# Optimization experiments

Measured on AMD Instinct MI355X. Metric: run time of the kernel, lower is better.

The kernel has to match this reference:

```python
import jax, jax.numpy as jnp
import numpy as np

H, HKV, D = 8, 1, 256  # query heads, kv heads, head_dim (Gemma-2B-like)


def apply_rope(x, sin, cos):
    # x: [B, h, D, S]; sin/cos: [B, 1, D//2, S]
    x1, x2 = jnp.split(x, 2, axis=-2)
    return jnp.concatenate((x1 * cos - x2 * sin, x2 * cos + x1 * sin), axis=-2)


def setup_inputs() -> dict:
    key = jax.random.key(0)
    ks = jax.random.split(key, 12)
    B, hidden, S = 2, 2048, 2048
    half = D // 2
    Xq = jax.random.normal(ks[0], (B, hidden, S), jnp.float32)
    Xkv = jax.random.normal(ks[1], (B, hidden, S), jnp.float32)
    sin_q = jax.random.uniform(ks[2], (B, 1, half, S), jnp.float32, -1.0, 1.0)
    cos_q = jax.random.uniform(ks[3], (B, 1, half, S), jnp.float32, -1.0, 1.0)
    sin_k = jax.random.uniform(ks[4], (B, 1, half, S), jnp.float32, -1.0, 1.0)
    cos_k = jax.random.uniform(ks[5], (B, 1, half, S), jnp.float32, -1.0, 1.0)
    attn_mask = jnp.zeros((B, 1, S, S), jnp.float32)
    scale = 0.02
    Wq = jax.random.normal(ks[6], (H * D, hidden), jnp.float32) * scale
    Wk = jax.random.normal(ks[7], (HKV * D, hidden), jnp.float32) * scale
    Wv = jax.random.normal(ks[8], (HKV * D, hidden), jnp.float32) * scale
    Wo = jax.random.normal(ks[9], (hidden, H * D), jnp.float32) * scale
    return {"Xq": Xq, "Xkv": Xkv, "sin_q": sin_q, "cos_q": cos_q,
            "sin_k": sin_k, "cos_k": cos_k, "attn_mask": attn_mask,
            "Wq": Wq, "Wk": Wk, "Wv": Wv, "Wo": Wo}


def reference(Xq, Xkv, sin_q, cos_q, sin_k, cos_k, attn_mask, Wq, Wk, Wv, Wo):
    B, hidden, Sq = Xq.shape
    Sk = Xkv.shape[-1]
    # ANEDenseGeneral = 1x1 conv over channels-first layout
    q = jnp.einsum('oc,bcs->bos', Wq, Xq).reshape(B, H, D, Sq)
    q = apply_rope(q, sin_q, cos_q)
    k = jnp.einsum('oc,bcs->bos', Wk, Xkv).reshape(B, HKV, D, Sk)
    k = apply_rope(k, sin_k, cos_k)
    v = jnp.einsum('oc,bcs->bos', Wv, Xkv).reshape(B, HKV, D, Sk)
    # GQA: broadcast kv heads to query heads
    rep = H // HKV
    k = jnp.repeat(k, rep, axis=1)
    v = jnp.repeat(v, rep, axis=1)
    scale = 1.0 / jnp.sqrt(jnp.asarray(D, Xq.dtype))
    scores = jnp.einsum('bhdq,bhdk->bhqk', q, k) * scale + attn_mask
    probs = jax.nn.softmax(scores, axis=-1)
    out = jnp.einsum('bhqk,bhdk->bhdq', probs, v).reshape(B, H * D, Sq)
    return jnp.einsum('oc,bcs->bos', Wo, out).astype(Xq.dtype)
```

## Files before the change

### kernel.cpp

```cpp
#include <hip/hip_runtime.h>

typedef __bf16 bf16;
typedef __bf16 bf16x8 __attribute__((ext_vector_type(8)));
typedef __bf16 bf16x4 __attribute__((ext_vector_type(4)));
typedef float f32x4 __attribute__((ext_vector_type(4)));

static constexpr int Hh = 8;
static constexpr int Dd = 256;
static constexpr int Ss = 2048;
static constexpr int Cc = 2048;
static constexpr int NS = 4096;

typedef const __attribute__((address_space(1))) unsigned int as1_u32;
typedef __attribute__((address_space(3))) unsigned int as3_u32;

__device__ __forceinline__ void gl_lds16(const void* g, void* l) {
  __builtin_amdgcn_global_load_lds((as1_u32*)(unsigned long long)g,
                                   (as3_u32*)(unsigned int)(unsigned long long)l,
                                   16, 0, 0);
}

__device__ __forceinline__ f32x4 mfma16(bf16x8 a, bf16x8 b, f32x4 c) {
  return __builtin_amdgcn_mfma_f32_16x16x32_bf16(a, b, c, 0, 0, 0);
}

__global__ __launch_bounds__(256) void cvt_w(const float* __restrict__ in,
                                             bf16* __restrict__ out, int n) {
  int i = (blockIdx.x * 256 + threadIdx.x) * 4;
  if (i >= n) return;
  const float4 v = *(const float4*)(in + i);
  bf16x4 o;
  o[0] = (bf16)v.x; o[1] = (bf16)v.y; o[2] = (bf16)v.z; o[3] = (bf16)v.w;
  *(bf16x4*)(out + i) = o;
}

__global__ __launch_bounds__(256) void transpose_cvt(const float* __restrict__ in,
                                                     bf16* __restrict__ out,
                                                     int R, int S) {
  __shared__ float t[32][33];
  const int b = blockIdx.z;
  const long base = (long)b * R * S;
  const int s0 = blockIdx.x * 32, r0 = blockIdx.y * 32;
  const int tx = threadIdx.x, ty = threadIdx.y;
#pragma unroll
  for (int i = 0; i < 32; i += 8)
    t[ty + i][tx] = in[base + (long)(r0 + ty + i) * S + s0 + tx];
  __syncthreads();
#pragma unroll
  for (int i = 0; i < 32; i += 8)
    out[base + (long)(s0 + ty + i) * R + r0 + tx] = (bf16)t[tx][ty + i];
}

__global__ __launch_bounds__(256) void transpose_cvt4(
    const float* __restrict__ s0, const float* __restrict__ s1,
    const float* __restrict__ s2, const float* __restrict__ s3,
    bf16* __restrict__ d0, bf16* __restrict__ d1, bf16* __restrict__ d2,
    bf16* __restrict__ d3, int R, int S) {
  __shared__ float t[32][33];
  const int arr = blockIdx.y >> 2;
  const int r0 = (blockIdx.y & 3) * 32;
  const float* in = (arr == 0) ? s0 : (arr == 1) ? s1 : (arr == 2) ? s2 : s3;
  bf16* out = (arr == 0) ? d0 : (arr == 1) ? d1 : (arr == 2) ? d2 : d3;
  const int b = blockIdx.z;
  const long base = (long)b * R * S;
  const int s0i = blockIdx.x * 32;
  const int tx = threadIdx.x, ty = threadIdx.y;
#pragma unroll
  for (int i = 0; i < 32; i += 8)
    t[ty + i][tx] = in[base + (long)(r0 + ty + i) * S + s0i + tx];
  __syncthreads();
#pragma unroll
  for (int i = 0; i < 32; i += 8)
    out[base + (long)(s0i + ty + i) * R + r0 + tx] = (bf16)t[tx][ty + i];
}

__global__ __launch_bounds__(256) void rope_transpose(
    const bf16* __restrict__ xin, const bf16* __restrict__ sint,
    const bf16* __restrict__ cost, bf16* __restrict__ xout, int nH,
    long bOff, long rowStr) {
  __shared__ __align__(16) bf16 ti[32][264];
  const int b = blockIdx.z, h = blockIdx.y, s0 = blockIdx.x * 32;
  const int tx = threadIdx.x, ty = threadIdx.y;
  const bf16* src = xin + b * bOff + (long)h * Dd * rowStr + s0;
#pragma unroll
  for (int i = 0; i < 32; ++i) {
    int d = ty + i * 8;
    ti[tx][d] = src[(long)d * rowStr + tx];
  }
  __syncthreads();
  const int t = ty * 32 + tx;
  const int s = t >> 3;
  const int dpart = t & 7;
  const bf16* sp = sint + ((long)b * Ss + s0 + s) * 128;
  const bf16* cp = cost + ((long)b * Ss + s0 + s) * 128;
  bf16* dst = xout + (((long)(b * nH + h)) * Ss + s0 + s) * Dd;
#pragma unroll
  for (int i = 0; i < 4; ++i) {
    int d0 = dpart * 8 + i * 64;
    int dh = d0 & 127;
    bf16x8 a = *(const bf16x8*)&ti[s][d0];
    bf16x8 p = *(const bf16x8*)&ti[s][(d0 < 128) ? d0 + 128 : d0 - 128];
    bf16x8 sn = *(const bf16x8*)&sp[dh];
    bf16x8 cs = *(const bf16x8*)&cp[dh];
    bf16x8 o;
#pragma unroll
    for (int j = 0; j < 8; ++j) {
      float av = (float)a[j], pv = (float)p[j];
      float c = (float)cs[j], sv = (float)sn[j];
      float val = (d0 < 128) ? (av * c - pv * sv) : (av * c + pv * sv);
      o[j] = (bf16)val;
    }
    *(bf16x8*)&dst[d0] = o;
  }
}

__global__ __launch_bounds__(256, 2) void gemm_bt(
    const bf16* __restrict__ A, const bf16* __restrict__ Bt,
    bf16* __restrict__ Cb, float* __restrict__ Cf, int M, int N, int K,
    int ntiles) {
  __shared__ __align__(16) bf16 lA[2][128 * 64];
  __shared__ __align__(16) bf16 lB[2][128 * 64];
  const int nwg = gridDim.x;
  const int cpx = nwg >> 3;
  const int bid2 = (blockIdx.x & 7) * cpx + (blockIdx.x >> 3);
  const int mt = (bid2 / ntiles) * 128, nt = (bid2 % ntiles) * 128;
  const int tid = threadIdx.x;
  const int wid = tid >> 6, lane = tid & 63;
  const int g = lane >> 4, r = lane & 15;
  const int wr = wid >> 1, wc = wid & 1;

  auto stage = [&](int buf, int kt) {
#pragma unroll
    for (int it = 0; it < 4; ++it) {
      int off = it * 4096 + tid * 16;
      int row = off >> 7;
      int c = (off >> 4) & 7;
      int csw = c ^ (row & 7);
      gl_lds16((const char*)(A + (long)(mt + row) * K + kt) + csw * 16,
               (char*)lA[buf] + it * 4096 + wid * 1024);
      gl_lds16((const char*)(Bt + (long)(nt + row) * K + kt) + csw * 16,
               (char*)lB[buf] + it * 4096 + wid * 1024);
    }
  };

  const f32x4 zf = {0.f, 0.f, 0.f, 0.f};
  f32x4 acc[4][4];
#pragma unroll
  for (int m = 0; m < 4; ++m)
#pragma unroll
    for (int n = 0; n < 4; ++n) acc[m][n] = zf;

  stage(0, 0);
  __syncthreads();
  int cur = 0;
  for (int kt = 0; kt < K; kt += 64) {
    if (kt + 64 < K) stage(cur ^ 1, kt + 64);
#pragma unroll
    for (int kk = 0; kk < 2; ++kk) {
      bf16x8 af[4], bfv[4];
#pragma unroll
      for (int m = 0; m < 4; ++m) {
        int row = wr * 64 + m * 16 + r;
        int csw = (kk * 4 + g) ^ (row & 7);
        af[m] = *(const bf16x8*)((const char*)lA[cur] + row * 128 + csw * 16);
      }
#pragma unroll
      for (int n = 0; n < 4; ++n) {
        int row = wc * 64 + n * 16 + r;
        int csw = (kk * 4 + g) ^ (row & 7);
        bfv[n] = *(const bf16x8*)((const char*)lB[cur] + row * 128 + csw * 16);
      }
#pragma unroll
      for (int m = 0; m < 4; ++m)
#pragma unroll
        for (int n = 0; n < 4; ++n)
          acc[m][n] = mfma16(af[m], bfv[n], acc[m][n]);
    }
    __syncthreads();
    cur ^= 1;
  }

#pragma unroll
  for (int m = 0; m < 4; ++m)
#pragma unroll
    for (int n = 0; n < 4; ++n)
#pragma unroll
      for (int e = 0; e < 4; ++e) {
        int orow = mt + wr * 64 + m * 16 + g * 4 + e;
        int col = nt + wc * 64 + n * 16 + r;
        if (Cf) {
          long idx = (long)(col >> 11) * ((long)Cc * Ss) + (long)orow * Ss +
                     (col & 2047);
          Cf[idx] = acc[m][n][e];
        } else {
          Cb[(long)orow * N + col] = (bf16)acc[m][n][e];
        }
      }
}

__global__ __launch_bounds__(256, 3) void gemm_bt64(
    const bf16* __restrict__ A, const bf16* __restrict__ Bt,
    bf16* __restrict__ Cb, int M, int N, int K, int ntiles) {
  __shared__ __align__(16) bf16 lA[2][64 * 64];
  __shared__ __align__(16) bf16 lB[2][128 * 64];
  const int nwg = gridDim.x;
  const int cpx = nwg >> 3;
  const int bid2 = (blockIdx.x & 7) * cpx + (blockIdx.x >> 3);
  const int mt = (bid2 / ntiles) * 64, nt = (bid2 % ntiles) * 128;
  const int tid = threadIdx.x;
  const int wid = tid >> 6, lane = tid & 63;
  const int g = lane >> 4, r = lane & 15;
  const int wn = wid;

  auto stage = [&](int buf, int kt) {
#pragma unroll
    for (int it = 0; it < 2; ++it) {
      int off = it * 4096 + tid * 16;
      int row = off >> 7;
      int c = (off >> 4) & 7;
      int csw = c ^ (row & 7);
      gl_lds16((const char*)(A + (long)(mt + row) * K + kt) + csw * 16,
               (char*)lA[buf] + it * 4096 + wid * 1024);
    }
#pragma unroll
    for (int it = 0; it < 4; ++it) {
      int off = it * 4096 + tid * 16;
      int row = off >> 7;
      int c = (off >> 4) & 7;
      int csw = c ^ (row & 7);
      gl_lds16((const char*)(Bt + (long)(nt + row) * K + kt) + csw * 16,
               (char*)lB[buf] + it * 4096 + wid * 1024);
    }
  };

  const f32x4 zf = {0.f, 0.f, 0.f, 0.f};
  f32x4 acc[4][2];
#pragma unroll
  for (int m = 0; m < 4; ++m)
#pragma unroll
    for (int n = 0; n < 2; ++n) acc[m][n] = zf;

  stage(0, 0);
  __syncthreads();
  int cur = 0;
  for (int kt = 0; kt < K; kt += 64) {
    if (kt + 64 < K) stage(cur ^ 1, kt + 64);
#pragma unroll
    for (int kk = 0; kk < 2; ++kk) {
      bf16x8 af[4], bfv[2];
#pragma unroll
      for (int m = 0; m < 4; ++m) {
        int row = m * 16 + r;
        int csw = (kk * 4 + g) ^ (row & 7);
        af[m] = *(const bf16x8*)((const char*)lA[cur] + row * 128 + csw * 16);
      }
#pragma unroll
      for (int n = 0; n < 2; ++n) {
        int row = wn * 32 + n * 16 + r;
        int csw = (kk * 4 + g) ^ (row & 7);
        bfv[n] = *(const bf16x8*)((const char*)lB[cur] + row * 128 + csw * 16);
      }
#pragma unroll
      for (int m = 0; m < 4; ++m)
#pragma unroll
        for (int n = 0; n < 2; ++n)
          acc[m][n] = mfma16(af[m], bfv[n], acc[m][n]);
    }
    __syncthreads();
    cur ^= 1;
  }

#pragma unroll
  for (int m = 0; m < 4; ++m)
#pragma unroll
    for (int n = 0; n < 2; ++n)
#pragma unroll
      for (int e = 0; e < 4; ++e) {
        int orow = mt + m * 16 + g * 4 + e;
        int col = nt + wn * 32 + n * 16 + r;
        Cb[(long)orow * N + col] = (bf16)acc[m][n][e];
      }
}

__global__ __launch_bounds__(256, 2) void attn_kernel(
    const bf16* __restrict__ qr, const bf16* __restrict__ kr,
    const bf16* __restrict__ kv, const float* __restrict__ mask,
    bf16* __restrict__ aout) {
  __shared__ __align__(16) bf16 lK[2][32 * 256];
  __shared__ __align__(16) bf16 lV[2][256 * 32];
  __shared__ __align__(16) bf16 lP[4][16 * 40];
  const int b = blockIdx.z, hg = blockIdx.y;
  const int q0 = blockIdx.x * 16;
  const int tid = threadIdx.x;
  const int wid = tid >> 6, lane = tid & 63;
  const int g = lane >> 4, q = lane & 15;
  const int h = hg * 4 + wid;

  bf16x8 qf[8];
  const bf16* qp = qr + (((long)(b * Hh + h)) * Ss + q0 + q) * Dd;
#pragma unroll
  for (int kk = 0; kk < 8; ++kk) qf[kk] = *(const bf16x8*)&qp[kk * 32 + g * 8];

  const f32x4 zf = {0.f, 0.f, 0.f, 0.f};
  f32x4 oacc[16];
#pragma unroll
  for (int i = 0; i < 16; ++i) oacc[i] = zf;
  float mrun = -3e38f, lrun = 0.f;

  const char* kb = (const char*)(kr + (long)b * Ss * Dd);
  const char* vb = (const char*)(kv + (long)256 * NS + (long)b * Ss);
  const float* mb = mask + (long)b * Ss * Ss;

  auto stage = [&](int buf, int kt) {
    const char* gK = kb + (long)kt * 512;
#pragma unroll
    for (int it = 0; it < 4; ++it) {
      int off = it * 4096 + tid * 16;
      int row = off >> 9;
      int c = (off >> 4) & 31;
      int csw = c ^ (row & 7);
      gl_lds16(gK + row * 512 + csw * 16,
               (char*)lK[buf] + it * 4096 + wid * 1024);
    }
#pragma unroll
    for (int it = 0; it < 4; ++it) {
      int off = it * 4096 + tid * 16;
      int row = off >> 6;
      int c = (off >> 4) & 3;
      int csw = c ^ ((row >> 1) & 3);
      gl_lds16(vb + (long)row * (NS * 2) + (long)kt * 2 + csw * 16,
               (char*)lV[buf] + it * 4096 + wid * 1024);
    }
  };

  stage(0, 0);
  __syncthreads();
  int cur = 0;

  for (int kt = 0; kt < Ss; kt += 32) {
    if (kt + 32 < Ss) stage(cur ^ 1, kt + 32);

    const float* mrow = mb + (long)(q0 + q) * Ss + kt;
    const float4 mv0 = *(const float4*)(mrow + 4 * g);
    const float4 mv1 = *(const float4*)(mrow + 16 + 4 * g);

    f32x4 sacc[2] = {zf, zf};
    __builtin_amdgcn_s_setprio(1);
#pragma unroll
    for (int kk = 0; kk < 8; ++kk) {
#pragma unroll
      for (int n = 0; n < 2; ++n) {
        int row = n * 16 + q;
        int csw = (kk * 4 + g) ^ (row & 7);
        bf16x8 kf = *(const bf16x8*)((const char*)lK[cur] + row * 512 + csw * 16);
        sacc[n] = mfma16(kf, qf[kk], sacc[n]);
      }
    }
    __builtin_amdgcn_s_setprio(0);

    float x[8];
    x[0] = sacc[0][0] * 0.0625f + mv0.x;
    x[1] = sacc[0][1] * 0.0625f + mv0.y;
    x[2] = sacc[0][2] * 0.0625f + mv0.z;
    x[3] = sacc[0][3] * 0.0625f + mv0.w;
    x[4] = sacc[1][0] * 0.0625f + mv1.x;
    x[5] = sacc[1][1] * 0.0625f + mv1.y;
    x[6] = sacc[1][2] * 0.0625f + mv1.z;
    x[7] = sacc[1][3] * 0.0625f + mv1.w;
    float mx = fmaxf(fmaxf(fmaxf(x[0], x[1]), fmaxf(x[2], x[3])),
                     fmaxf(fmaxf(x[4], x[5]), fmaxf(x[6], x[7])));
    mx = fmaxf(mx, __shfl_xor(mx, 16, 64));
    mx = fmaxf(mx, __shfl_xor(mx, 32, 64));
    if (mx > mrun + 8.0f) {
      float al = __expf(mrun - mx);
      lrun *= al;
#pragma unroll
      for (int nf = 0; nf < 16; ++nf) oacc[nf] *= al;
      mrun = mx;
    }
    float p[8];
    float rs = 0.f;
#pragma unroll
    for (int i = 0; i < 8; ++i) {
      p[i] = __expf(x[i] - mrun);
      rs += p[i];
    }
    rs += __shfl_xor(rs, 16, 64);
    rs += __shfl_xor(rs, 32, 64);
    lrun += rs;

    bf16x4 w0, w1;
#pragma unroll
    for (int e = 0; e < 4; ++e) { w0[e] = (bf16)p[e]; w1[e] = (bf16)p[4 + e]; }
    *(bf16x4*)&lP[wid][q * 40 + 4 * g] = w0;
    *(bf16x4*)&lP[wid][q * 40 + 16 + 4 * g] = w1;

    bf16x8 pf = *(const bf16x8*)&lP[wid][q * 40 + g * 8];
    __builtin_amdgcn_s_setprio(1);
#pragma unroll
    for (int nf = 0; nf < 16; ++nf) {
      int row = nf * 16 + q;
      int csw = g ^ ((row >> 1) & 3);
      bf16x8 vf = *(const bf16x8*)((const char*)lV[cur] + row * 64 + csw * 16);
      oacc[nf] = mfma16(vf, pf, oacc[nf]);
    }
    __builtin_amdgcn_s_setprio(0);

    __syncthreads();
    cur ^= 1;
  }

  const float inv = 1.f / lrun;
  bf16* op = aout + ((long)(b * Ss + q0 + q)) * (Hh * Dd) + h * Dd + g * 4;
#pragma unroll
  for (int nf = 0; nf < 16; ++nf) {
    bf16x4 o4;
#pragma unroll
    for (int e = 0; e < 4; ++e) o4[e] = (bf16)(oacc[nf][e] * inv);
    *(bf16x4*)&op[nf * 16] = o4;
  }
}

extern "C" void kernel_launch(void* const* d_in, const int* in_sizes, int n_in,
                              void* d_out, int out_size, void* d_ws,
                              size_t ws_size, hipStream_t stream) {
  const float* Xq = (const float*)d_in[0];
  const float* Xkv = (const float*)d_in[1];
  const float* sin_q = (const float*)d_in[2];
  const float* cos_q = (const float*)d_in[3];
  const float* sin_k = (const float*)d_in[4];
  const float* cos_k = (const float*)d_in[5];
  const float* mask = (const float*)d_in[6];
  const float* Wq = (const float*)d_in[7];
  const float* Wk = (const float*)d_in[8];
  const float* Wv = (const float*)d_in[9];
  const float* Wo = (const float*)d_in[10];
  float* out = (float*)d_out;

  char* ws = (char*)d_ws;
  const size_t MB = 1u << 20;
  bf16* Wq_bf = (bf16*)(ws + 0 * MB);
  bf16* Wo_bf = (bf16*)(ws + 8 * MB);
  bf16* Wkv_bf = (bf16*)(ws + 16 * MB);
  bf16* Wv_bf = (bf16*)(ws + 17 * MB);
  bf16* sin_qt = (bf16*)(ws + 18 * MB);
  bf16* cos_qt = (bf16*)(ws + 19 * MB);
  bf16* sin_kt = (bf16*)(ws + 20 * MB);
  bf16* cos_kt = (bf16*)(ws + 21 * MB);
  bf16* Xtq = (bf16*)(ws + 22 * MB);
  bf16* Xtkv = (bf16*)(ws + 38 * MB);
  bf16* q_tmp = (bf16*)(ws + 54 * MB);
  bf16* kv_tmp = (bf16*)(ws + 70 * MB);
  bf16* qr = (bf16*)(ws + 22 * MB);
  bf16* kr = (bf16*)(ws + 38 * MB);
  bf16* attnb = (bf16*)(ws + 54 * MB);

  dim3 b256(256), b32x8(32, 8);

  cvt_w<<<4096, b256, 0, stream>>>(Wq, Wq_bf, Cc * Cc);
  cvt_w<<<4096, b256, 0, stream>>>(Wo, Wo_bf, Cc * Cc);
  cvt_w<<<512, b256, 0, stream>>>(Wk, (bf16*)Wkv_bf, Dd * Cc);
  cvt_w<<<512, b256, 0, stream>>>(Wv, Wv_bf, Dd * Cc);

  transpose_cvt<<<dim3(64, 64, 2), b32x8, 0, stream>>>(Xq, Xtq, Cc, Ss);
  transpose_cvt<<<dim3(64, 64, 2), b32x8, 0, stream>>>(Xkv, Xtkv, Cc, Ss);
  transpose_cvt4<<<dim3(64, 16, 2), b32x8, 0, stream>>>(
      sin_q, cos_q, sin_k, cos_k, sin_qt, cos_qt, sin_kt, cos_kt, 128, Ss);

  gemm_bt<<<dim3(512), b256, 0, stream>>>(Wq_bf, Xtq, q_tmp, nullptr,
                                          Cc, NS, Cc, NS / 128);
  gemm_bt64<<<dim3(256), b256, 0, stream>>>(Wkv_bf, Xtkv, kv_tmp,
                                            2 * Dd, NS, Cc, NS / 128);

  rope_transpose<<<dim3(64, 8, 2), b32x8, 0, stream>>>(
      q_tmp, sin_qt, cos_qt, qr, Hh, (long)Ss, (long)NS);
  rope_transpose<<<dim3(64, 1, 2), b32x8, 0, stream>>>(
      kv_tmp, sin_kt, cos_kt, kr, 1, (long)Ss, (long)NS);

  attn_kernel<<<dim3(128, 2, 2), b256, 0, stream>>>(qr, kr, kv_tmp, mask,
                                                    attnb);

  gemm_bt<<<dim3(512), b256, 0, stream>>>(Wo_bf, attnb, nullptr, out,
                                          Cc, NS, Cc, NS / 128);
}
```

Measured before the change: 278.9 us.

## Split attention over KV halves with merge kernel and 32x32 MFMA

The attention kernel now splits each query tile's key range into two halves, each handled by its own block, and writes partial outputs plus running max and sum. A new merge kernel combines the two halves. The kernel also moves from 16x16x32 to 32x32x16 MFMA with 32-query tiles. The P matrix now stays in registers via permlane32 swaps instead of going through LDS. Block indices are swizzled to spread work. The online-softmax rescale is now unconditional. This adds a merge pass and extra partial-output traffic (the output buffer is reused as scratch) in exchange for more parallelism and fewer LDS round trips.

```diff
diff --git a/kernel.cpp b/kernel.cpp
--- a/kernel.cpp
+++ b/kernel.cpp
@@ -3,7 +3,11 @@
 typedef __bf16 bf16;
 typedef __bf16 bf16x8 __attribute__((ext_vector_type(8)));
 typedef __bf16 bf16x4 __attribute__((ext_vector_type(4)));
+typedef __bf16 bf16x2 __attribute__((ext_vector_type(2)));
 typedef float f32x4 __attribute__((ext_vector_type(4)));
+typedef float f32x16 __attribute__((ext_vector_type(16)));
+typedef unsigned u32;
+typedef unsigned u32x4v __attribute__((ext_vector_type(4)));
 
 static constexpr int Hh = 8;
 static constexpr int Dd = 256;
@@ -22,6 +26,16 @@
 
 __device__ __forceinline__ f32x4 mfma16(bf16x8 a, bf16x8 b, f32x4 c) {
   return __builtin_amdgcn_mfma_f32_16x16x32_bf16(a, b, c, 0, 0, 0);
+}
+__device__ __forceinline__ f32x16 mfma32(bf16x8 a, bf16x8 b, f32x16 c) {
+  return __builtin_amdgcn_mfma_f32_32x32x16_bf16(a, b, c, 0, 0, 0);
+}
+
+__device__ __forceinline__ u32 pk_bf16(float lo, float hi) {
+  bf16x2 t;
+  t[0] = (bf16)lo;
+  t[1] = (bf16)hi;
+  return __builtin_bit_cast(u32, t);
 }
 
 __global__ __launch_bounds__(256) void cvt_w(const float* __restrict__ in,
@@ -282,29 +296,31 @@
       }
 }
 
-__global__ __launch_bounds__(256, 2) void attn_kernel(
+__global__ __launch_bounds__(256, 2) void attn_split(
     const bf16* __restrict__ qr, const bf16* __restrict__ kr,
     const bf16* __restrict__ kv, const float* __restrict__ mask,
-    bf16* __restrict__ aout) {
+    bf16* __restrict__ opart, float2* __restrict__ ml) {
   __shared__ __align__(16) bf16 lK[2][32 * 256];
   __shared__ __align__(16) bf16 lV[2][256 * 32];
-  __shared__ __align__(16) bf16 lP[4][16 * 40];
-  const int b = blockIdx.z, hg = blockIdx.y;
-  const int q0 = blockIdx.x * 16;
+  const int i = blockIdx.x;
+  const int flat = (i & 7) * 64 + (i >> 3);
+  const int b = flat >> 8;
+  const int rem = flat & 255;
+  const int kvh = rem >> 7;
+  const int hg = (rem >> 6) & 1;
+  const int q0 = (rem & 63) * 32;
   const int tid = threadIdx.x;
   const int wid = tid >> 6, lane = tid & 63;
-  const int g = lane >> 4, q = lane & 15;
+  const int l31 = lane & 31, hi = lane >> 5;
   const int h = hg * 4 + wid;
 
-  bf16x8 qf[8];
-  const bf16* qp = qr + (((long)(b * Hh + h)) * Ss + q0 + q) * Dd;
-#pragma unroll
-  for (int kk = 0; kk < 8; ++kk) qf[kk] = *(const bf16x8*)&qp[kk * 32 + g * 8];
-
-  const f32x4 zf = {0.f, 0.f, 0.f, 0.f};
-  f32x4 oacc[16];
-#pragma unroll
-  for (int i = 0; i < 16; ++i) oacc[i] = zf;
+  bf16x8 qf[16];
+  const bf16* qp = qr + (((long)(b * Hh + h)) * Ss + q0 + l31) * Dd;
+#pragma unroll
+  for (int kk = 0; kk < 16; ++kk)
+    qf[kk] = *(const bf16x8*)&qp[kk * 16 + hi * 8];
+
+  f32x16 oacc[8] = {};
   float mrun = -3e38f, lrun = 0.f;
 
   const char* kb = (const char*)(kr + (long)b * Ss * Dd);
@@ -333,76 +349,79 @@
     }
   };
 
-  stage(0, 0);
+  const int kbeg = kvh * (Ss / 2), kend = kbeg + (Ss / 2);
+  stage(0, kbeg);
   __syncthreads();
   int cur = 0;
 
-  for (int kt = 0; kt < Ss; kt += 32) {
-    if (kt + 32 < Ss) stage(cur ^ 1, kt + 32);
-
-    const float* mrow = mb + (long)(q0 + q) * Ss + kt;
-    const float4 mv0 = *(const float4*)(mrow + 4 * g);
-    const float4 mv1 = *(const float4*)(mrow + 16 + 4 * g);
-
-    f32x4 sacc[2] = {zf, zf};
+  for (int kt = kbeg; kt < kend; kt += 32) {
+    if (kt + 32 < kend) stage(cur ^ 1, kt + 32);
+
+    const float* mrow = mb + (long)(q0 + l31) * Ss + kt;
+    float4 mv[4];
+#pragma unroll
+    for (int grp = 0; grp < 4; ++grp)
+      mv[grp] = *(const float4*)(mrow + grp * 8 + hi * 4);
+
+    f32x16 sacc = {};
     __builtin_amdgcn_s_setprio(1);
 #pragma unroll
-    for (int kk = 0; kk < 8; ++kk) {
-#pragma unroll
-      for (int n = 0; n < 2; ++n) {
-        int row = n * 16 + q;
-        int csw = (kk * 4 + g) ^ (row & 7);
-        bf16x8 kf = *(const bf16x8*)((const char*)lK[cur] + row * 512 + csw * 16);
-        sacc[n] = mfma16(kf, qf[kk], sacc[n]);
-      }
+    for (int kk = 0; kk < 16; ++kk) {
+      int csw = (kk * 2 + hi) ^ (l31 & 7);
+      bf16x8 kf = *(const bf16x8*)((const char*)lK[cur] + l31 * 512 + csw * 16);
+      sacc = mfma32(kf, qf[kk], sacc);
     }
     __builtin_amdgcn_s_setprio(0);
 
-    float x[8];
-    x[0] = sacc[0][0] * 0.0625f + mv0.x;
-    x[1] = sacc[0][1] * 0.0625f + mv0.y;
-    x[2] = sacc[0][2] * 0.0625f + mv0.z;
-    x[3] = sacc[0][3] * 0.0625f + mv0.w;
-    x[4] = sacc[1][0] * 0.0625f + mv1.x;
-    x[5] = sacc[1][1] * 0.0625f + mv1.y;
-    x[6] = sacc[1][2] * 0.0625f + mv1.z;
-    x[7] = sacc[1][3] * 0.0625f + mv1.w;
-    float mx = fmaxf(fmaxf(fmaxf(x[0], x[1]), fmaxf(x[2], x[3])),
-                     fmaxf(fmaxf(x[4], x[5]), fmaxf(x[6], x[7])));
-    mx = fmaxf(mx, __shfl_xor(mx, 16, 64));
+    float x[16];
+#pragma unroll
+    for (int r = 0; r < 16; ++r)
+      x[r] = sacc[r] * 0.0625f + ((const float*)&mv[r >> 2])[r & 3];
+    float mx = fmaxf(
+        fmaxf(fmaxf(fmaxf(x[0], x[1]), fmaxf(x[2], x[3])),
+              fmaxf(fmaxf(x[4], x[5]), fmaxf(x[6], x[7]))),
+        fmaxf(fmaxf(fmaxf(x[8], x[9]), fmaxf(x[10], x[11])),
+              fmaxf(fmaxf(x[12], x[13]), fmaxf(x[14], x[15]))));
     mx = fmaxf(mx, __shfl_xor(mx, 32, 64));
-    if (mx > mrun + 8.0f) {
-      float al = __expf(mrun - mx);
-      lrun *= al;
-#pragma unroll
-      for (int nf = 0; nf < 16; ++nf) oacc[nf] *= al;
-      mrun = mx;
-    }
-    float p[8];
-    float rs = 0.f;
-#pragma unroll
-    for (int i = 0; i < 8; ++i) {
-      p[i] = __expf(x[i] - mrun);
-      rs += p[i];
-    }
-    rs += __shfl_xor(rs, 16, 64);
+    const float mnew = fmaxf(mrun, mx);
+    const float al = __expf(mrun - mnew);
+    mrun = mnew;
+    float p[16];
+#pragma unroll
+    for (int r = 0; r < 16; ++r) p[r] = __expf(x[r] - mrun);
+    float rs = ((p[0] + p[1]) + (p[2] + p[3])) +
+               ((p[4] + p[5]) + (p[6] + p[7])) +
+               ((p[8] + p[9]) + (p[10] + p[11])) +
+               ((p[12] + p[13]) + (p[14] + p[15]));
     rs += __shfl_xor(rs, 32, 64);
-    lrun += rs;
-
-    bf16x4 w0, w1;
-#pragma unroll
-    for (int e = 0; e < 4; ++e) { w0[e] = (bf16)p[e]; w1[e] = (bf16)p[4 + e]; }
-    *(bf16x4*)&lP[wid][q * 40 + 4 * g] = w0;
-    *(bf16x4*)&lP[wid][q * 40 + 16 + 4 * g] = w1;
-
-    bf16x8 pf = *(const bf16x8*)&lP[wid][q * 40 + g * 8];
+    lrun = lrun * al + rs;
+#pragma unroll
+    for (int d = 0; d < 8; ++d) oacc[d] *= al;
+
+    bf16x8 pf[2];
+#pragma unroll
+    for (int kk2 = 0; kk2 < 2; ++kk2) {
+      u32 a0 = pk_bf16(p[kk2 * 8 + 0], p[kk2 * 8 + 1]);
+      u32 a1 = pk_bf16(p[kk2 * 8 + 2], p[kk2 * 8 + 3]);
+      u32 b0 = pk_bf16(p[kk2 * 8 + 4], p[kk2 * 8 + 5]);
+      u32 b1 = pk_bf16(p[kk2 * 8 + 6], p[kk2 * 8 + 7]);
+      asm("v_permlane32_swap_b32 %0, %1" : "+v"(a0), "+v"(b0));
+      asm("v_permlane32_swap_b32 %0, %1" : "+v"(a1), "+v"(b1));
+      u32x4v w;
+      w[0] = a0; w[1] = a1; w[2] = b0; w[3] = b1;
+      pf[kk2] = __builtin_bit_cast(bf16x8, w);
+    }
+
     __builtin_amdgcn_s_setprio(1);
 #pragma unroll
-    for (int nf = 0; nf < 16; ++nf) {
-      int row = nf * 16 + q;
-      int csw = g ^ ((row >> 1) & 3);
-      bf16x8 vf = *(const bf16x8*)((const char*)lV[cur] + row * 64 + csw * 16);
-      oacc[nf] = mfma16(vf, pf, oacc[nf]);
+    for (int kk2 = 0; kk2 < 2; ++kk2) {
+#pragma unroll
+      for (int db = 0; db < 8; ++db) {
+        int csw = (kk2 * 2 + hi) ^ ((l31 >> 1) & 3);
+        bf16x8 vf = *(const bf16x8*)((const char*)lV[cur] +
+                                     (db * 32 + l31) * 64 + csw * 16);
+        oacc[db] = mfma32(vf, pf[kk2], oacc[db]);
+      }
     }
     __builtin_amdgcn_s_setprio(0);
 
@@ -411,13 +430,56 @@
   }
 
   const float inv = 1.f / lrun;
-  bf16* op = aout + ((long)(b * Ss + q0 + q)) * (Hh * Dd) + h * Dd + g * 4;
-#pragma unroll
-  for (int nf = 0; nf < 16; ++nf) {
-    bf16x4 o4;
-#pragma unroll
-    for (int e = 0; e < 4; ++e) o4[e] = (bf16)(oacc[nf][e] * inv);
-    *(bf16x4*)&op[nf * 16] = o4;
+  const long ridx = (((long)(b * 2 + kvh) * Hh + h)) * Ss + q0 + l31;
+  bf16* po = opart + ridx * Dd;
+#pragma unroll
+  for (int db = 0; db < 8; ++db) {
+#pragma unroll
+    for (int grp = 0; grp < 4; ++grp) {
+      bf16x4 o4;
+#pragma unroll
+      for (int e = 0; e < 4; ++e) o4[e] = (bf16)(oacc[db][grp * 4 + e] * inv);
+      *(bf16x4*)&po[db * 32 + grp * 8 + hi * 4] = o4;
+    }
+  }
+  if (hi == 0) {
+    float2 v;
+    v.x = mrun;
+    v.y = lrun;
+    ml[ridx] = v;
+  }
+}
+
+__global__ __launch_bounds__(256) void attn_merge(
+    const bf16* __restrict__ opart, const float2* __restrict__ ml,
+    bf16* __restrict__ attnb) {
+  const long t = (long)blockIdx.x * 256 + threadIdx.x;
+  const int d0 = (int)(t & 7) << 5;
+  const long R = t >> 3;
+  const long b = R >> 14;
+  const long rem = R & 16383;
+  const int h = (int)(rem >> 11);
+  const int s = (int)(rem & 2047);
+  const long i0 = (b * 2 + 0) * ((long)Hh * Ss) + rem;
+  const long i1 = (b * 2 + 1) * ((long)Hh * Ss) + rem;
+  const float2 ml0 = ml[i0], ml1 = ml[i1];
+  const float m = fmaxf(ml0.x, ml1.x);
+  const float w0 = ml0.y * __expf(ml0.x - m);
+  const float w1 = ml1.y * __expf(ml1.x - m);
+  const float inv = 1.f / (w0 + w1);
+  const float s0 = w0 * inv, s1 = w1 * inv;
+  const bf16* p0 = opart + i0 * Dd + d0;
+  const bf16* p1 = opart + i1 * Dd + d0;
+  bf16* po = attnb + ((long)b * Ss + s) * (Hh * Dd) + h * Dd + d0;
+#pragma unroll
+  for (int j = 0; j < 4; ++j) {
+    bf16x8 v0 = *(const bf16x8*)(p0 + j * 8);
+    bf16x8 v1 = *(const bf16x8*)(p1 + j * 8);
+    bf16x8 o;
+#pragma unroll
+    for (int e = 0; e < 8; ++e)
+      o[e] = (bf16)((float)v0[e] * s0 + (float)v1[e] * s1);
+    *(bf16x8*)(po + j * 8) = o;
   }
 }
 
@@ -449,11 +511,13 @@
   bf16* cos_kt = (bf16*)(ws + 21 * MB);
   bf16* Xtq = (bf16*)(ws + 22 * MB);
   bf16* Xtkv = (bf16*)(ws + 38 * MB);
+  float2* ml = (float2*)(ws + 44 * MB);
   bf16* q_tmp = (bf16*)(ws + 54 * MB);
   bf16* kv_tmp = (bf16*)(ws + 70 * MB);
   bf16* qr = (bf16*)(ws + 22 * MB);
   bf16* kr = (bf16*)(ws + 38 * MB);
   bf16* attnb = (bf16*)(ws + 54 * MB);
+  bf16* opart = (bf16*)d_out;
 
   dim3 b256(256), b32x8(32, 8);
 
@@ -477,8 +541,8 @@
   rope_transpose<<<dim3(64, 1, 2), b32x8, 0, stream>>>(
       kv_tmp, sin_kt, cos_kt, kr, 1, (long)Ss, (long)NS);
 
-  attn_kernel<<<dim3(128, 2, 2), b256, 0, stream>>>(qr, kr, kv_tmp, mask,
-                                                    attnb);
+  attn_split<<<dim3(512), b256, 0, stream>>>(qr, kr, kv_tmp, mask, opart, ml);
+  attn_merge<<<dim3(1024), b256, 0, stream>>>(opart, ml, attnb);
 
   gemm_bt<<<dim3(512), b256, 0, stream>>>(Wo_bf, attnb, nullptr, out,
                                           Cc, NS, Cc, NS / 128);
```

Result: slower. 314.8 us (+12.9%).
